# Optimization experiments

Measured on AMD Instinct MI355X. Metric: run time of the kernel, lower is better.

Reference implementation:

```python
import jax, jax.numpy as jnp
import numpy as np

N = 8192       # n_concepts
D = 128        # embed_dim
L = 2          # n_layers
ALPHA = 0.7
BETA = 0.3
LAM = 0.1      # lambda_decay


def setup_inputs() -> dict:
    key = jax.random.key(0)
    ks = jax.random.split(key, 16)
    adj = jax.random.randint(ks[0], (N, N), 0, 2).astype(jnp.float32)
    s = 0.05
    return {
        "adj": adj,
        "concept_embed": jax.random.normal(ks[1], (N, D), jnp.float32) * s,
        # torch Linear weight is [out,in]; stored here as [in,out] for x @ W
        "gc_w": jax.random.normal(ks[2], (L, D, D), jnp.float32) * s,
        "gc_b": jnp.zeros((L, D), jnp.float32),
        "wq": jax.random.normal(ks[3], (D, D), jnp.float32) * s,
        "bq": jnp.zeros((D,), jnp.float32),
        "wk": jax.random.normal(ks[4], (D, D), jnp.float32) * s,
        "bk": jnp.zeros((D,), jnp.float32),
        "wv": jax.random.normal(ks[5], (D, D), jnp.float32) * s,
        "bv": jnp.zeros((D,), jnp.float32),
        "g1_w": jax.random.normal(ks[6], (4 * D, 2 * D), jnp.float32) * s,
        "g1_b": jnp.zeros((2 * D,), jnp.float32),
        "g2_w": jax.random.normal(ks[7], (2 * D, 4), jnp.float32) * s,
        "g2_b": jnp.zeros((4,), jnp.float32),
        "layer_weights": jnp.ones((L,), jnp.float32) / L,
    }


def _aggregate(E, adj, wq, bq, wk, bk, wv, bv, g1_w, g1_b, g2_w, g2_b):
    nbr = adj != 0                                            # [N,N] neighbor pattern
    nrm = jnp.maximum(jnp.linalg.norm(E, axis=1), 1e-8)       # torch cosine_similarity eps
    sim = (E @ E.T) / (nrm[:, None] * nrm[None, :])           # [N,N] cosine sims
    pos = nbr & (sim >= ALPHA)
    neg = nbr & (sim <= BETA)
    bnd = nbr & (sim > BETA) & (sim < ALPHA)
    posf = pos.astype(E.dtype)
    negf = neg.astype(E.dtype)
    # masked means (zero when region empty, matching torch zeros fallback)
    pos_emb = (posf @ E) / jnp.maximum(posf.sum(1, keepdims=True), 1.0)
    neg_emb = LAM * (negf @ E) / jnp.maximum(negf.sum(1, keepdims=True), 1.0)
    # boundary region: attention of node i over its boundary neighbors
    Q = E @ wq + bq
    K = E @ wk + bk
    V = E @ wv + bv
    s = (Q @ K.T) / np.sqrt(D).astype(np.float32)             # [N,N]
    m = jnp.max(jnp.where(bnd, s, -jnp.inf), axis=1, keepdims=True)
    m = jnp.where(jnp.isfinite(m), m, 0.0)                    # safe max when region empty
    e = jnp.where(bnd, jnp.exp(s - m), 0.0)
    w = e / jnp.maximum(e.sum(1, keepdims=True), 1e-30)       # masked softmax (0 if empty)
    bnd_emb = w @ V
    # gated fusion of [self, pos, bound, neg]
    concat = jnp.concatenate([E, pos_emb, bnd_emb, neg_emb], axis=1)  # [N,4D]
    h = jax.nn.relu(concat @ g1_w + g1_b)
    gate = jax.nn.softmax(h @ g2_w + g2_b, axis=-1)           # [N,4]
    regions = jnp.stack([E, pos_emb, bnd_emb, neg_emb], axis=1)  # [N,4,D]
    fused = jnp.einsum('nr,nrd->nd', gate, regions)
    # nodes with no neighbors keep their own embedding
    return jnp.where(nbr.any(axis=1, keepdims=True), fused, E)


def reference(adj, concept_embed, gc_w, gc_b, wq, bq, wk, bk, wv, bv,
              g1_w, g1_b, g2_w, g2_b, layer_weights):
    cur = concept_embed
    outs = []
    for l in range(L):
        agg = _aggregate(cur, adj, wq, bq, wk, bk, wv, bv, g1_w, g1_b, g2_w, g2_b)
        cur = jax.nn.relu(agg @ gc_w[l] + gc_b[l])
        outs.append(cur)
    lw = jax.nn.softmax(layer_weights)
    return jnp.einsum('l,lnd->nd', lw, jnp.stack(outs))
```

## Files before the change

kernel.cpp:

```cpp
#include <hip/hip_runtime.h>
#include <stdint.h>

#define NN 8192
#define DD 128
#define ALPHA 0.7f
#define BETA 0.3f
#define LAM 0.1f
#define QSCALE 0.08838834764831845f
#define DELTA 3e-5f
#define FLAGCAP 262144
#define FLAG2CAP 1048576

typedef __attribute__((ext_vector_type(8))) short short8;
typedef __attribute__((ext_vector_type(4))) float f32x4;
typedef unsigned short ush;

__device__ __forceinline__ ush f2bf(float f){
  union { float f; unsigned u; } v; v.f = f;
  return (ush)((v.u + 0x7FFFu + ((v.u >> 16) & 1u)) >> 16);
}
__device__ __forceinline__ float bf2f(ush s){
  union { unsigned u; float f; } v; v.u = ((unsigned)s) << 16; return v.f;
}

__global__ void k_pack(const float* __restrict__ adj, unsigned* __restrict__ adjw){
  int i = blockIdx.x, wave = threadIdx.x >> 6, lane = threadIdx.x & 63;
  for (int seg = wave; seg < 128; seg += 4){
    int j = seg*64 + lane;
    unsigned long long bm = __ballot(adj[(size_t)i*NN + j] != 0.0f);
    if (lane == 0)  adjw[i*256 + seg*2]     = (unsigned)bm;
    if (lane == 32) adjw[i*256 + seg*2 + 1] = (unsigned)(bm >> 32);
  }
}

__global__ void k_norm(const float* __restrict__ E, double* __restrict__ nrm64,
                       ush* __restrict__ Enh, ush* __restrict__ Enl){
  int i = blockIdx.x*4 + (threadIdx.x >> 6);
  int l = threadIdx.x & 63;
  float v0 = E[i*DD + l], v1 = E[i*DD + 64 + l];
  double ss = (double)v0*(double)v0 + (double)v1*(double)v1;
  #pragma unroll
  for (int m = 32; m; m >>= 1) ss += __shfl_xor(ss, m, 64);
  double nr = sqrt(ss); if (nr < 1e-8) nr = 1e-8;
  float inv = (float)(1.0 / nr);
  float n0 = v0*inv, n1 = v1*inv;
  ush h0 = f2bf(n0), h1 = f2bf(n1);
  Enh[i*DD + l] = h0;       Enh[i*DD + 64 + l] = h1;
  Enl[i*DD + l] = f2bf(n0 - bf2f(h0));
  Enl[i*DD + 64 + l] = f2bf(n1 - bf2f(h1));
  if (l == 0) nrm64[i] = nr;
}

__global__ void k_transsplit(const float* __restrict__ in, ush* __restrict__ outH,
                             ush* __restrict__ outL){
  __shared__ float t[64][65];
  int r0 = blockIdx.x * 64, c0 = blockIdx.y * 64;
  for (int idx = threadIdx.x; idx < 4096; idx += 256){
    int r = idx >> 6, c = idx & 63;
    t[r][c] = in[(r0 + r)*DD + c0 + c];
  }
  __syncthreads();
  for (int idx = threadIdx.x; idx < 4096; idx += 256){
    int c = idx >> 6, r = idx & 63;
    float v = t[r][c];
    ush h = f2bf(v);
    outH[(size_t)(c0 + c)*NN + r0 + r] = h;
    outL[(size_t)(c0 + c)*NN + r0 + r] = f2bf(v - bf2f(h));
  }
}

__global__ void k_transw_all(const float* __restrict__ wq, const float* __restrict__ wk,
                             const float* __restrict__ wv, const float* __restrict__ g1w,
                             const float* __restrict__ gcw,
                             ush* __restrict__ qkvTh, ush* __restrict__ qkvTl,
                             ush* __restrict__ g1wTh, ush* __restrict__ g1wTl,
                             ush* __restrict__ gcwTh, ush* __restrict__ gcwTl){
  int idx = blockIdx.x*256 + threadIdx.x;
  const float* src; ush *dh, *dl; int K, Nout, li;
  if      (idx <  16384){ src=wq;        dh=qkvTh;        dl=qkvTl;        K=128; Nout=128; li=idx; }
  else if (idx <  32768){ src=wk;        dh=qkvTh+16384;  dl=qkvTl+16384;  K=128; Nout=128; li=idx-16384; }
  else if (idx <  49152){ src=wv;        dh=qkvTh+32768;  dl=qkvTl+32768;  K=128; Nout=128; li=idx-32768; }
  else if (idx < 180224){ src=g1w;       dh=g1wTh;        dl=g1wTl;        K=512; Nout=256; li=idx-49152; }
  else if (idx < 196608){ src=gcw;       dh=gcwTh;        dl=gcwTl;        K=128; Nout=128; li=idx-180224; }
  else if (idx < 212992){ src=gcw+16384; dh=gcwTh+16384;  dl=gcwTl+16384;  K=128; Nout=128; li=idx-196608; }
  else return;
  int k = li / Nout, n = li - k*Nout;
  float v = src[li];
  ush h = f2bf(v);
  dh[n*K + k] = h;
  dl[n*K + k] = f2bf(v - bf2f(h));
}

__global__ void k_qkv(const float* __restrict__ A,
                      const ush* __restrict__ BtH, const ush* __restrict__ BtL,
                      const float* __restrict__ bq, const float* __restrict__ bk,
                      const float* __restrict__ bv,
                      ush* __restrict__ Qh, ush* __restrict__ Kh,
                      ush* __restrict__ VhT, ush* __restrict__ VloT){
  __shared__ float sV[128*33];
  int tid = threadIdx.x, lane = tid & 63, wave = tid >> 6;
  int l15 = lane & 15, quad = lane >> 4;
  int rowblk = blockIdx.x * 32;
  int row16 = rowblk + (wave >> 1)*16;
  int nf0 = (wave & 1)*12;
  f32x4 acc[12];
  #pragma unroll
  for (int i = 0; i < 12; i++){ f32x4 z = {0.f,0.f,0.f,0.f}; acc[i] = z; }
  #pragma unroll
  for (int kk = 0; kk < 4; kk++){
    const float* ap = &A[(row16 + l15)*DD + kk*32 + quad*8];
    short8 ah, al;
    #pragma unroll
    for (int j = 0; j < 8; j++){
      float v = ap[j];
      ush h = f2bf(v);
      ah[j] = (short)h; al[j] = (short)f2bf(v - bf2f(h));
    }
    #pragma unroll
    for (int i = 0; i < 12; i++){
      int bo = ((nf0 + i)*16 + l15)*DD + kk*32 + quad*8;
      short8 bh = *(const short8*)&BtH[bo];
      short8 bl = *(const short8*)&BtL[bo];
      acc[i] = __builtin_amdgcn_mfma_f32_16x16x32_bf16(ah, bh, acc[i], 0, 0, 0);
      acc[i] = __builtin_amdgcn_mfma_f32_16x16x32_bf16(al, bh, acc[i], 0, 0, 0);
      acc[i] = __builtin_amdgcn_mfma_f32_16x16x32_bf16(ah, bl, acc[i], 0, 0, 0);
    }
  }
  #pragma unroll
  for (int i = 0; i < 12; i++){
    int nfg = nf0 + i;
    int grp = nfg >> 3;
    int col = (nfg & 7)*16 + l15;
    float b = (grp == 0) ? bq[col] : (grp == 1) ? bk[col] : bv[col];
    #pragma unroll
    for (int r = 0; r < 4; r++){
      int row = row16 + quad*4 + r;
      float v = acc[i][r] + b;
      if (grp == 0)      Qh[row*DD + col] = f2bf(v * QSCALE);
      else if (grp == 1) Kh[row*DD + col] = f2bf(v);
      else               sV[col*33 + (row - rowblk)] = v;
    }
  }
  __syncthreads();
  int feat = tid >> 1, rh = (tid & 1)*16;
  ush hh[16], ll[16];
  #pragma unroll
  for (int j = 0; j < 16; j++){
    float v = sV[feat*33 + rh + j];
    ush h = f2bf(v);
    hh[j] = h; ll[j] = f2bf(v - bf2f(h));
  }
  size_t go = (size_t)feat*NN + rowblk + rh;
  *(uint4*)&VhT [go]     = *(const uint4*)&hh[0];
  *(uint4*)&VhT [go + 8] = *(const uint4*)&hh[8];
  *(uint4*)&VloT[go]     = *(const uint4*)&ll[0];
  *(uint4*)&VloT[go + 8] = *(const uint4*)&ll[8];
}

__global__ void k_g1(const float* __restrict__ E, const float* __restrict__ P,
                     const float* __restrict__ B, const float* __restrict__ N,
                     const float* __restrict__ cntP, const float* __restrict__ cntN,
                     const float* __restrict__ denB,
                     const ush* __restrict__ BtH, const ush* __restrict__ BtL,
                     const float* __restrict__ bias, float* __restrict__ out){
  int tid = threadIdx.x, lane = tid & 63, wave = tid >> 6;
  int l15 = lane & 15, quad = lane >> 4;
  int row16 = blockIdx.x*16;
  int nf0 = wave*4;
  int row = row16 + l15;
  float cp = cntP[row], cn = cntN[row], dn = denB[row];
  float rs[4] = {1.f, 1.f/fmaxf(cp,1.f), (dn > 0.5f) ? (1.f/dn) : 0.f, LAM/fmaxf(cn,1.f)};
  const float* bases[4] = {E, P, B, N};
  f32x4 acc[4];
  #pragma unroll
  for (int nf = 0; nf < 4; nf++){ f32x4 z = {0.f,0.f,0.f,0.f}; acc[nf] = z; }
  #pragma unroll
  for (int kk = 0; kk < 16; kk++){
    const float* ap = &bases[kk>>2][row*DD + (kk&3)*32 + quad*8];
    float sc = rs[kk>>2];
    short8 ah, al;
    #pragma unroll
    for (int j = 0; j < 8; j++){
      float v = ap[j] * sc;
      ush h = f2bf(v);
      ah[j] = (short)h; al[j] = (short)f2bf(v - bf2f(h));
    }
    #pragma unroll
    for (int nf = 0; nf < 4; nf++){
      int bo = ((nf0 + nf)*16 + l15)*512 + kk*32 + quad*8;
      short8 bh = *(const short8*)&BtH[bo];
      short8 bl = *(const short8*)&BtL[bo];
      acc[nf] = __builtin_amdgcn_mfma_f32_16x16x32_bf16(ah, bh, acc[nf], 0, 0, 0);
      acc[nf] = __builtin_amdgcn_mfma_f32_16x16x32_bf16(al, bh, acc[nf], 0, 0, 0);
      acc[nf] = __builtin_amdgcn_mfma_f32_16x16x32_bf16(ah, bl, acc[nf], 0, 0, 0);
    }
  }
  #pragma unroll
  for (int nf = 0; nf < 4; nf++){
    int col = (nf0 + nf)*16 + l15;
    float b = bias[col];
    #pragma unroll
    for (int r = 0; r < 4; r++){
      int rr = row16 + quad*4 + r;
      out[rr*256 + col] = fmaxf(acc[nf][r] + b, 0.f);
    }
  }
}

__global__ void k_fusegc(const float* __restrict__ E, const float* __restrict__ P,
                         const float* __restrict__ B, const float* __restrict__ N,
                         const float* __restrict__ hbuf, const float* __restrict__ g2w,
                         const float* __restrict__ g2b,
                         const float* __restrict__ cntP, const float* __restrict__ cntN,
                         const float* __restrict__ denB,
                         const ush* __restrict__ BtH, const ush* __restrict__ BtL,
                         const float* __restrict__ bias,
                         const float* __restrict__ prevC, const float* __restrict__ lwv,
                         int dofinal, float* __restrict__ out){
  int tid = threadIdx.x, lane = tid & 63, wave = tid >> 6;
  int l15 = lane & 15, quad = lane >> 4;
  int row16 = blockIdx.x*16;
  int nf0 = wave*2;
  int row = row16 + l15;
  float l0=0,l1=0,l2=0,l3=0;
  #pragma unroll
  for (int i = 0; i < 16; i++){
    float4 hv = *(const float4*)&hbuf[row*256 + quad*64 + i*4];
    float hvv[4] = {hv.x, hv.y, hv.z, hv.w};
    #pragma unroll
    for (int j = 0; j < 4; j++){
      float4 w4 = *(const float4*)&g2w[(quad*64 + i*4 + j)*4];
      l0 = fmaf(hvv[j], w4.x, l0); l1 = fmaf(hvv[j], w4.y, l1);
      l2 = fmaf(hvv[j], w4.z, l2); l3 = fmaf(hvv[j], w4.w, l3);
    }
  }
  l0 += __shfl_xor(l0,16,64); l0 += __shfl_xor(l0,32,64);
  l1 += __shfl_xor(l1,16,64); l1 += __shfl_xor(l1,32,64);
  l2 += __shfl_xor(l2,16,64); l2 += __shfl_xor(l2,32,64);
  l3 += __shfl_xor(l3,16,64); l3 += __shfl_xor(l3,32,64);
  l0 += g2b[0]; l1 += g2b[1]; l2 += g2b[2]; l3 += g2b[3];
  float mx = fmaxf(fmaxf(l0,l1), fmaxf(l2,l3));
  float e0 = __expf(l0-mx), e1 = __expf(l1-mx), e2 = __expf(l2-mx), e3 = __expf(l3-mx);
  float inv = 1.f/(e0+e1+e2+e3);
  float g0 = e0*inv, g1v = e1*inv, g2v = e2*inv, g3 = e3*inv;
  float cp = cntP[row], cn = cntN[row], dn = denB[row];
  bool any = (cp + cn > 0.5f) || (dn > 0.5f);
  float pscl = g1v/fmaxf(cp,1.f);
  float bscl = (dn > 0.5f) ? (g2v/dn) : 0.f;
  float nscl = LAM*g3/fmaxf(cn,1.f);
  f32x4 acc[2];
  #pragma unroll
  for (int nf = 0; nf < 2; nf++){ f32x4 z = {0.f,0.f,0.f,0.f}; acc[nf] = z; }
  #pragma unroll
  for (int kk = 0; kk < 4; kk++){
    int koff = row*DD + kk*32 + quad*8;
    short8 ah, al;
    #pragma unroll
    for (int j = 0; j < 8; j++){
      float ev = E[koff + j];
      float v = any ? (g0*ev + pscl*P[koff+j] + bscl*B[koff+j] + nscl*N[koff+j]) : ev;
      ush h = f2bf(v);
      ah[j] = (short)h; al[j] = (short)f2bf(v - bf2f(h));
    }
    #pragma unroll
    for (int nf = 0; nf < 2; nf++){
      int bo = ((nf0 + nf)*16 + l15)*DD + kk*32 + quad*8;
      short8 bh = *(const short8*)&BtH[bo];
      short8 bl = *(const short8*)&BtL[bo];
      acc[nf] = __builtin_amdgcn_mfma_f32_16x16x32_bf16(ah, bh, acc[nf], 0, 0, 0);
      acc[nf] = __builtin_amdgcn_mfma_f32_16x16x32_bf16(al, bh, acc[nf], 0, 0, 0);
      acc[nf] = __builtin_amdgcn_mfma_f32_16x16x32_bf16(ah, bl, acc[nf], 0, 0, 0);
    }
  }
  float we0 = 0.5f, we1 = 0.5f;
  if (dofinal){
    float a0 = lwv[0], a1 = lwv[1];
    float mw = fmaxf(a0, a1);
    float x0 = __expf(a0-mw), x1 = __expf(a1-mw);
    float iv = 1.f/(x0+x1);
    we0 = x0*iv; we1 = x1*iv;
  }
  #pragma unroll
  for (int nf = 0; nf < 2; nf++){
    int col = (nf0 + nf)*16 + l15;
    float b = bias[col];
    #pragma unroll
    for (int r = 0; r < 4; r++){
      int rr = row16 + quad*4 + r;
      float val = fmaxf(acc[nf][r] + b, 0.f);
      if (dofinal) val = we0*prevC[rr*DD + col] + we1*val;
      out[rr*DD + col] = val;
    }
  }
}

#define BM 64
#define BN 32
#define CSPLIT 4
#define CCHUNK (NN/CSPLIT)
#define NTILES (CCHUNK/BN)
#define RSTRIDE 136
#define FSTRIDE 80
#define MSTRIDE 80

template<int DENSEB>
__launch_bounds__(256, 2)
__global__ void k_fused(const unsigned* __restrict__ adjw,
    const ush* __restrict__ Enh, const ush* __restrict__ Enl,
    const ush* __restrict__ Qh,  const ush* __restrict__ Kh,
    const ush* __restrict__ EhiT, const ush* __restrict__ EloT,
    const ush* __restrict__ VhT,  const ush* __restrict__ VloT,
    float* __restrict__ Nsum, float* __restrict__ Bsum,
    float* __restrict__ cntN, float* __restrict__ denB,
    int* __restrict__ flagCnt, float4* __restrict__ flags,
    int* __restrict__ flag2Cnt, float4* __restrict__ flags2)
{
  __shared__ __attribute__((aligned(16))) ush sEnh[32*RSTRIDE];
  __shared__ __attribute__((aligned(16))) ush sEnl[32*RSTRIDE];
  __shared__ __attribute__((aligned(16))) ush sKh [32*RSTRIDE];
  __shared__ __attribute__((aligned(16))) ush sE2 [128*FSTRIDE];
  __shared__ __attribute__((aligned(16))) ush sV2 [DENSEB ? 128*FSTRIDE : 16];
  __shared__ __attribute__((aligned(16))) ush sM  [4][16*MSTRIDE];

  int tid = threadIdx.x, lane = tid & 63, wave = tid >> 6;
  int l15 = lane & 15, quad = lane >> 4;
  int rowblk = blockIdx.x >> 2, split = blockIdx.x & 3;
  int row0 = rowblk * BM + wave * 16;
  int col0 = split * CCHUNK;

  short8 bEnh[4], bEnl[4], bQ[4];
  #pragma unroll
  for (int kf = 0; kf < 4; kf++){
    int go = (row0 + l15)*DD + kf*32 + quad*8;
    bEnh[kf] = *(const short8*)&Enh[go];
    bEnl[kf] = *(const short8*)&Enl[go];
    bQ  [kf] = *(const short8*)&Qh [go];
  }

  f32x4 accN[8], accB[DENSEB ? 8 : 1];
  #pragma unroll
  for (int nf = 0; nf < 8; nf++){ f32x4 z = {0.f,0.f,0.f,0.f}; accN[nf]=z; }
  if (DENSEB){
    #pragma unroll
    for (int nf = 0; nf < 8; nf++){ f32x4 z = {0.f,0.f,0.f,0.f}; accB[nf]=z; }
  }
  float cnL = 0.f, dbL = 0.f;

  int f0 = tid >> 2,        n0 = (tid & 3)*8;
  int f1 = (tid+256) >> 2,  n1 = ((tid+256) & 3)*8;
  uint4 pEh0, pEh1, pEl0, pEl1, pVh0, pVh1, pVl0, pVl1;
  {
    size_t g0 = (size_t)f0*NN + col0 + n0, g1 = (size_t)f1*NN + col0 + n1;
    pEh0 = *(const uint4*)&EhiT[g0]; pEh1 = *(const uint4*)&EhiT[g1];
    pEl0 = *(const uint4*)&EloT[g0]; pEl1 = *(const uint4*)&EloT[g1];
    if (DENSEB){
      pVh0 = *(const uint4*)&VhT [g0]; pVh1 = *(const uint4*)&VhT [g1];
      pVl0 = *(const uint4*)&VloT[g0]; pVl1 = *(const uint4*)&VloT[g1];
    }
  }
  int rr0 = tid >> 4,       ro0 = (tid & 15)*8;
  int rr1 = (tid+256) >> 4, ro1 = ((tid+256) & 15)*8;

  for (int t = 0; t < NTILES; t++){
    int c0 = col0 + t*BN;
    __syncthreads();
    *(uint4*)&sE2[f0*FSTRIDE + n0]      = pEh0;  *(uint4*)&sE2[f1*FSTRIDE + n1]      = pEh1;
    *(uint4*)&sE2[f0*FSTRIDE + 40 + n0] = pEl0;  *(uint4*)&sE2[f1*FSTRIDE + 40 + n1] = pEl1;
    if (DENSEB){
      *(uint4*)&sV2[f0*FSTRIDE + n0]      = pVh0;  *(uint4*)&sV2[f1*FSTRIDE + n1]      = pVh1;
      *(uint4*)&sV2[f0*FSTRIDE + 40 + n0] = pVl0;  *(uint4*)&sV2[f1*FSTRIDE + 40 + n1] = pVl1;
    }
    {
      uint4 a0 = *(const uint4*)&Enh[(c0 + rr0)*DD + ro0];
      uint4 a1 = *(const uint4*)&Enh[(c0 + rr1)*DD + ro1];
      uint4 b0 = *(const uint4*)&Enl[(c0 + rr0)*DD + ro0];
      uint4 b1 = *(const uint4*)&Enl[(c0 + rr1)*DD + ro1];
      uint4 k0 = *(const uint4*)&Kh [(c0 + rr0)*DD + ro0];
      uint4 k1 = *(const uint4*)&Kh [(c0 + rr1)*DD + ro1];
      *(uint4*)&sEnh[rr0*RSTRIDE + ro0] = a0;  *(uint4*)&sEnh[rr1*RSTRIDE + ro1] = a1;
      *(uint4*)&sEnl[rr0*RSTRIDE + ro0] = b0;  *(uint4*)&sEnl[rr1*RSTRIDE + ro1] = b1;
      *(uint4*)&sKh [rr0*RSTRIDE + ro0] = k0;  *(uint4*)&sKh [rr1*RSTRIDE + ro1] = k1;
    }
    __syncthreads();
    if (t + 1 < NTILES){
      int c1 = c0 + BN;
      size_t g0 = (size_t)f0*NN + c1 + n0, g1 = (size_t)f1*NN + c1 + n1;
      pEh0 = *(const uint4*)&EhiT[g0]; pEh1 = *(const uint4*)&EhiT[g1];
      pEl0 = *(const uint4*)&EloT[g0]; pEl1 = *(const uint4*)&EloT[g1];
      if (DENSEB){
        pVh0 = *(const uint4*)&VhT [g0]; pVh1 = *(const uint4*)&VhT [g1];
        pVl0 = *(const uint4*)&VloT[g0]; pVl1 = *(const uint4*)&VloT[g1];
      }
    }
    unsigned aw = adjw[(row0 + l15)*256 + (c0 >> 5)];

    f32x4 simT[2], svT[2];
    { f32x4 z = {0.f,0.f,0.f,0.f}; simT[0]=z; simT[1]=z; svT[0]=z; svT[1]=z; }
    #pragma unroll
    for (int f = 0; f < 2; f++){
      #pragma unroll
      for (int kf = 0; kf < 4; kf++){
        int la = (f*16 + l15)*RSTRIDE + kf*32 + quad*8;
        short8 ch = *(const short8*)&sEnh[la];
        short8 cl = *(const short8*)&sEnl[la];
        short8 ck = *(const short8*)&sKh [la];
        simT[f] = __builtin_amdgcn_mfma_f32_16x16x32_bf16(ch, bEnh[kf], simT[f],0,0,0);
        simT[f] = __builtin_amdgcn_mfma_f32_16x16x32_bf16(cl, bEnh[kf], simT[f],0,0,0);
        simT[f] = __builtin_amdgcn_mfma_f32_16x16x32_bf16(ch, bEnl[kf], simT[f],0,0,0);
        svT [f] = __builtin_amdgcn_mfma_f32_16x16x32_bf16(ck, bQ  [kf], svT [f],0,0,0);
      }
    }
    ushort4 ehv[2], elv[2];
    unsigned flagb = 0, spb = 0;
    #pragma unroll
    for (int f = 0; f < 2; f++){
      ush vn2[4], veh[4], vel[4];
      #pragma unroll
      for (int r = 0; r < 4; r++){
        int cbit = f*16 + quad*4 + r;
        bool nbr = (aw >> cbit) & 1u;
        float c = simT[f][r], s = svT[f][r];
        bool pos = nbr && (c >= ALPHA);
        bool neg = nbr && (c <= BETA);
        bool bnd = nbr && !pos && !neg;
        vn2[r] = neg ? (ush)0x3F80 : (ush)0;
        cnL += neg ? 1.f : 0.f;
        if (DENSEB){
          float e = bnd ? __expf(s) : 0.f;
          ush eh = f2bf(e);
          veh[r] = eh;
          vel[r] = f2bf(e - bf2f(eh));
          dbL += e;
        }
        if (nbr && (fabsf(c - ALPHA) < DELTA || fabsf(c - BETA) < DELTA))
          flagb |= 1u << (f*4 + r);
        if (pos || (!DENSEB && bnd))
          spb |= 1u << (f*4 + r);
      }
      int mb = l15*MSTRIDE + f*16 + quad*4;
      *(ushort4*)&sM[wave][mb] = make_ushort4(vn2[0],vn2[1],vn2[2],vn2[3]);
      if (DENSEB){
        ehv[f] = make_ushort4(veh[0],veh[1],veh[2],veh[3]);
        elv[f] = make_ushort4(vel[0],vel[1],vel[2],vel[3]);
      }
    }
    if (__ballot((flagb | spb) != 0)){
      #pragma unroll
      for (int f = 0; f < 2; f++){
        #pragma unroll
        for (int r = 0; r < 4; r++){
          int bit = f*4 + r;
          bool fl = (flagb >> bit) & 1u;
          unsigned long long bm = __ballot(fl);
          if (bm){
            int leader = __ffsll((long long)bm) - 1;
            int base = 0;
            if (lane == leader) base = atomicAdd(flagCnt, __popcll(bm));
            base = __shfl(base, leader, 64);
            if (fl){
              int id = base + __popcll(bm & ((1ull << lane) - 1ull));
              if (id < FLAGCAP){
                float4 rec;
                rec.x = __int_as_float(row0 + l15);
                rec.y = __int_as_float(c0 + f*16 + quad*4 + r);
                rec.z = simT[f][r]; rec.w = svT[f][r];
                flags[id] = rec;
              }
            }
          }
          bool f2 = (spb >> bit) & 1u;
          unsigned long long bm2 = __ballot(f2);
          if (bm2){
            int leader = __ffsll((long long)bm2) - 1;
            int base = 0;
            if (lane == leader) base = atomicAdd(flag2Cnt, __popcll(bm2));
            base = __shfl(base, leader, 64);
            if (f2){
              int id = base + __popcll(bm2 & ((1ull << lane) - 1ull));
              if (id < FLAG2CAP){
                float c = simT[f][r];
                int j = c0 + f*16 + quad*4 + r;
                int cls = (c >= ALPHA) ? 0 : 1;
                float4 rec;
                rec.x = __int_as_float(row0 + l15);
                rec.y = __int_as_float(j | (cls << 16));
                rec.z = c; rec.w = svT[f][r];
                flags2[id] = rec;
              }
            }
          }
        }
      }
    }
    {
      short8 mNeg = *(const short8*)&sM[wave][l15*MSTRIDE + quad*8];
      #pragma unroll
      for (int nf = 0; nf < 8; nf++){
        int so = (nf*16 + l15)*FSTRIDE + quad*8;
        short8 eth = *(const short8*)&sE2[so];
        short8 etl = *(const short8*)&sE2[so + 40];
        accN[nf] = __builtin_amdgcn_mfma_f32_16x16x32_bf16(mNeg, eth, accN[nf],0,0,0);
        accN[nf] = __builtin_amdgcn_mfma_f32_16x16x32_bf16(mNeg, etl, accN[nf],0,0,0);
      }
    }
    if (DENSEB){
      int mb0 = l15*MSTRIDE + quad*4;
      *(ushort4*)&sM[wave][mb0]      = ehv[0];
      *(ushort4*)&sM[wave][mb0 + 16] = ehv[1];
      *(ushort4*)&sM[wave][mb0 + 40] = elv[0];
      *(ushort4*)&sM[wave][mb0 + 56] = elv[1];
      short8 mEh = *(const short8*)&sM[wave][l15*MSTRIDE + quad*8];
      short8 mEl = *(const short8*)&sM[wave][l15*MSTRIDE + 40 + quad*8];
      #pragma unroll
      for (int nf = 0; nf < 8; nf++){
        int so = (nf*16 + l15)*FSTRIDE + quad*8;
        short8 vth = *(const short8*)&sV2[so];
        short8 vtl = *(const short8*)&sV2[so + 40];
        accB[nf] = __builtin_amdgcn_mfma_f32_16x16x32_bf16(mEh, vth, accB[nf],0,0,0);
        accB[nf] = __builtin_amdgcn_mfma_f32_16x16x32_bf16(mEl, vth, accB[nf],0,0,0);
        accB[nf] = __builtin_amdgcn_mfma_f32_16x16x32_bf16(mEh, vtl, accB[nf],0,0,0);
      }
    }
  }
  #pragma unroll
  for (int nf = 0; nf < 8; nf++){
    int col = nf*16 + l15;
    #pragma unroll
    for (int r = 0; r < 4; r++){
      int row = row0 + quad*4 + r;
      atomicAdd(&Nsum[row*DD + col], accN[nf][r]);
      if (DENSEB) atomicAdd(&Bsum[row*DD + col], accB[nf][r]);
    }
  }
  cnL += __shfl_xor(cnL, 16, 64); cnL += __shfl_xor(cnL, 32, 64);
  if (DENSEB){ dbL += __shfl_xor(dbL, 16, 64); dbL += __shfl_xor(dbL, 32, 64); }
  if (quad == 0){
    atomicAdd(&cntN[row0 + l15], cnL);
    if (DENSEB) atomicAdd(&denB[row0 + l15], dbL);
  }
}

__global__ void k_sparsePB(const ush* __restrict__ EhiT, const ush* __restrict__ EloT,
    const ush* __restrict__ VhT,  const ush* __restrict__ VloT,
    const int* __restrict__ flag2Cnt, const float4* __restrict__ flags2,
    float* __restrict__ Psum, float* __restrict__ Bsum,
    float* __restrict__ cntP, float* __restrict__ denB)
{
  int cnt = *flag2Cnt; if (cnt > FLAG2CAP) cnt = FLAG2CAP;
  int lane = threadIdx.x & 63;
  int gw = (blockIdx.x * blockDim.x + threadIdx.x) >> 6;
  int nw = (gridDim.x * blockDim.x) >> 6;
  for (int idx = gw; idx < cnt; idx += nw){
    float4 rec = flags2[idx];
    int i = __float_as_int(rec.x);
    int jraw = __float_as_int(rec.y);
    int j = jraw & 0xFFFF, cls = jraw >> 16;
    if (cls == 0){
      #pragma unroll
      for (int h = 0; h < 2; h++){
        int d = lane + h*64;
        float ev = bf2f(EhiT[(size_t)d*NN + j]) + bf2f(EloT[(size_t)d*NN + j]);
        atomicAdd(&Psum[i*DD + d], ev);
      }
      if (lane == 0) atomicAdd(&cntP[i], 1.f);
    } else {
      float e = __expf(rec.w);
      float ehf = bf2f(f2bf(e));
      float elf = bf2f(f2bf(e - ehf));
      #pragma unroll
      for (int h = 0; h < 2; h++){
        int d = lane + h*64;
        float vh = bf2f(VhT [(size_t)d*NN + j]);
        float vl = bf2f(VloT[(size_t)d*NN + j]);
        atomicAdd(&Bsum[i*DD + d], ehf*vh + elf*vh + ehf*vl);
      }
      if (lane == 0) atomicAdd(&denB[i], e);
    }
  }
}

__global__ void k_refine(const float* __restrict__ E, const double* __restrict__ nrm64,
    const ush* __restrict__ EhiT, const ush* __restrict__ EloT,
    const ush* __restrict__ VhT,  const ush* __restrict__ VloT,
    const int* __restrict__ flagCnt, const float4* __restrict__ flags,
    float* __restrict__ Psum, float* __restrict__ Nsum, float* __restrict__ Bsum,
    float* __restrict__ cntP, float* __restrict__ cntN, float* __restrict__ denB)
{
  int cnt = *flagCnt; if (cnt > FLAGCAP) cnt = FLAGCAP;
  int lane = threadIdx.x & 63;
  int gw = (blockIdx.x * blockDim.x + threadIdx.x) >> 6;
  int nw = (gridDim.x * blockDim.x) >> 6;
  for (int idx = gw; idx < cnt; idx += nw){
    float4 rec = flags[idx];
    int i = __float_as_int(rec.x), j = __float_as_int(rec.y);
    float c = rec.z, s = rec.w;
    float ei0 = E[i*DD + lane], ei1 = E[i*DD + 64 + lane];
    float ej0 = E[j*DD + lane], ej1 = E[j*DD + 64 + lane];
    double d = (double)ei0*(double)ej0 + (double)ei1*(double)ej1;
    #pragma unroll
    for (int m = 32; m; m >>= 1) d += __shfl_xor(d, m, 64);
    double se = d / (nrm64[i]*nrm64[j]);
    int ce = (se >= (double)ALPHA) ? 0 : ((se <= (double)BETA) ? 1 : 2);
    int cc = (c >= ALPHA) ? 0 : ((c <= BETA) ? 1 : 2);
    if (ce == cc) continue;
    float e = __expf(s);
    float ehf = bf2f(f2bf(e));
    float elf = bf2f(f2bf(e - ehf));
    #pragma unroll
    for (int h = 0; h < 2; h++){
      int dd2 = lane + h*64;
      float ev = bf2f(EhiT[(size_t)dd2*NN + j]) + bf2f(EloT[(size_t)dd2*NN + j]);
      float vh = bf2f(VhT[(size_t)dd2*NN + j]);
      float vl = bf2f(VloT[(size_t)dd2*NN + j]);
      float bv = ehf*vh + elf*vh + ehf*vl;
      float* subA = (cc==0) ? Psum : (cc==1) ? Nsum : Bsum;
      atomicAdd(&subA[i*DD + dd2], (cc==2) ? -bv : -ev);
      float* addA = (ce==0) ? Psum : (ce==1) ? Nsum : Bsum;
      atomicAdd(&addA[i*DD + dd2], (ce==2) ?  bv :  ev);
    }
    if (lane == 0){
      float* subC = (cc==0) ? cntP : (cc==1) ? cntN : denB;
      atomicAdd(&subC[i], (cc==2) ? -e : -1.f);
      float* addC = (ce==0) ? cntP : (ce==1) ? cntN : denB;
      atomicAdd(&addC[i], (ce==2) ?  e :  1.f);
    }
  }
}

extern "C" void kernel_launch(void* const* d_in, const int* in_sizes, int n_in,
                              void* d_out, int out_size, void* d_ws, size_t ws_size,
                              hipStream_t stream){
  const float* adj   = (const float*)d_in[0];
  const float* embed = (const float*)d_in[1];
  const float* gc_w  = (const float*)d_in[2];
  const float* gc_b  = (const float*)d_in[3];
  const float* wq = (const float*)d_in[4];
  const float* bq = (const float*)d_in[5];
  const float* wk = (const float*)d_in[6];
  const float* bk = (const float*)d_in[7];
  const float* wv = (const float*)d_in[8];
  const float* bv = (const float*)d_in[9];
  const float* g1w = (const float*)d_in[10];
  const float* g1b = (const float*)d_in[11];
  const float* g2w = (const float*)d_in[12];
  const float* g2b = (const float*)d_in[13];
  const float* lw  = (const float*)d_in[14];
  float* out = (float*)d_out;

  char* p = (char*)d_ws;
  auto alloc = [&](size_t bytes)->void*{ void* r = (void*)p; p += (bytes + 255) & ~(size_t)255; return r; };
  ush* qkvTh = (ush*)alloc(384*128*2);  ush* qkvTl = (ush*)alloc(384*128*2);
  ush* g1wTh = (ush*)alloc(512*256*2);  ush* g1wTl = (ush*)alloc(512*256*2);
  ush* gcwTh = (ush*)alloc(2*128*128*2); ush* gcwTl = (ush*)alloc(2*128*128*2);
  unsigned* adjw = (unsigned*)alloc((size_t)NN*256*4);
  double* nrm64 = (double*)alloc(NN*8);
  ush* Enh  = (ush*)alloc((size_t)NN*DD*2);
  ush* Enl  = (ush*)alloc((size_t)NN*DD*2);
  ush* EhiT = (ush*)alloc((size_t)NN*DD*2);
  ush* EloT = (ush*)alloc((size_t)NN*DD*2);
  ush* Qh   = (ush*)alloc((size_t)NN*DD*2);
  ush* Khb  = (ush*)alloc((size_t)NN*DD*2);
  ush* VhT  = (ush*)alloc((size_t)NN*DD*2);
  ush* VloT = (ush*)alloc((size_t)NN*DD*2);
  char* zbase = p;
  float* Psum = (float*)alloc((size_t)NN*DD*4);
  float* Nsum = (float*)alloc((size_t)NN*DD*4);
  float* Bsum = (float*)alloc((size_t)NN*DD*4);
  float* cntP = (float*)alloc(NN*4);
  float* cntN = (float*)alloc(NN*4);
  float* denB = (float*)alloc(NN*4);
  int*   flagCnt  = (int*)alloc(256);
  int*   flag2Cnt = (int*)alloc(256);
  size_t zbytes = (size_t)(p - zbase);
  float4* flags  = (float4*)alloc((size_t)FLAGCAP*16);
  float4* flags2 = (float4*)alloc((size_t)FLAG2CAP*16);
  float* hbuf = (float*)alloc((size_t)NN*256*4);
  float* cur0 = (float*)alloc((size_t)NN*DD*4);

  k_pack<<<NN, 256, 0, stream>>>(adj, adjw);
  k_transw_all<<<832, 256, 0, stream>>>(wq, wk, wv, g1w, gc_w,
      qkvTh, qkvTl, g1wTh, g1wTl, gcwTh, gcwTl);

  const float* Ecur = embed;
  for (int l = 0; l < 2; l++){
    k_norm<<<2048, 256, 0, stream>>>(Ecur, nrm64, Enh, Enl);
    k_transsplit<<<dim3(128,2), 256, 0, stream>>>(Ecur, EhiT, EloT);
    k_qkv<<<256, 256, 0, stream>>>(Ecur, qkvTh, qkvTl, bq, bk, bv, Qh, Khb, VhT, VloT);
    hipMemsetAsync(zbase, 0, zbytes, stream);
    if (l == 0)
      k_fused<0><<<(NN/BM)*CSPLIT, 256, 0, stream>>>(adjw, Enh, Enl, Qh, Khb,
          EhiT, EloT, VhT, VloT, Nsum, Bsum, cntN, denB,
          flagCnt, flags, flag2Cnt, flags2);
    else
      k_fused<1><<<(NN/BM)*CSPLIT, 256, 0, stream>>>(adjw, Enh, Enl, Qh, Khb,
          EhiT, EloT, VhT, VloT, Nsum, Bsum, cntN, denB,
          flagCnt, flags, flag2Cnt, flags2);
    k_sparsePB<<<256, 256, 0, stream>>>(EhiT, EloT, VhT, VloT, flag2Cnt, flags2,
        Psum, Bsum, cntP, denB);
    k_refine<<<512, 256, 0, stream>>>(Ecur, nrm64, EhiT, EloT, VhT, VloT, flagCnt, flags,
        Psum, Nsum, Bsum, cntP, cntN, denB);
    k_g1<<<512, 256, 0, stream>>>(Ecur, Psum, Bsum, Nsum, cntP, cntN, denB,
        g1wTh, g1wTl, g1b, hbuf);
    k_fusegc<<<512, 256, 0, stream>>>(Ecur, Psum, Bsum, Nsum, hbuf, g2w, g2b,
        cntP, cntN, denB, gcwTh + l*128*128, gcwTl + l*128*128, gc_b + l*128,
        cur0, lw, l, (l == 0) ? cur0 : out);
    Ecur = (l == 0) ? cur0 : out;
  }
}
```

Baseline: 1.111 ms.

## Merge prep, sparse-fix, and MLP kernels to cut launches and intermediate buffers

Three groups of kernels are combined into single launches. Norm, transpose-split and QKV become one k_prep dispatched by block index. The sparse P/B accumulation and the refine pass become one k_fix. The gate MLP (g1) and the fuse/gc stage become one k_mlp, which keeps the hidden activations in shared memory instead of a global hbuf. A dotmode flag also lets k_fix recompute the QK score from Q and K in layer 0 instead of using the stored value, which changes how the k_fused side stores records. The aim is fewer launches and less global traffic. The cost is larger heterogeneous blocks with more register and LDS pressure.

```diff
diff --git a/kernel.cpp b/kernel.cpp
--- a/kernel.cpp
+++ b/kernel.cpp
@@ -23,6 +23,17 @@
   union { unsigned u; float f; } v; v.u = ((unsigned)s) << 16; return v.f;
 }
 
+__device__ __forceinline__ float qkdot(const ush* __restrict__ Qh,
+                                       const ush* __restrict__ Kh,
+                                       int i, int j, int lane){
+  float q0 = bf2f(Qh[i*DD + lane]),      k0 = bf2f(Kh[j*DD + lane]);
+  float q1 = bf2f(Qh[i*DD + 64 + lane]), k1 = bf2f(Kh[j*DD + 64 + lane]);
+  float s = q0*k0 + q1*k1;
+  #pragma unroll
+  for (int m = 32; m; m >>= 1) s += __shfl_xor(s, m, 64);
+  return s;
+}
+
 __global__ void k_pack(const float* __restrict__ adj, unsigned* __restrict__ adjw){
   int i = blockIdx.x, wave = threadIdx.x >> 6, lane = threadIdx.x & 63;
   for (int seg = wave; seg < 128; seg += 4){
@@ -30,42 +41,6 @@
     unsigned long long bm = __ballot(adj[(size_t)i*NN + j] != 0.0f);
     if (lane == 0)  adjw[i*256 + seg*2]     = (unsigned)bm;
     if (lane == 32) adjw[i*256 + seg*2 + 1] = (unsigned)(bm >> 32);
-  }
-}
-
-__global__ void k_norm(const float* __restrict__ E, double* __restrict__ nrm64,
-                       ush* __restrict__ Enh, ush* __restrict__ Enl){
-  int i = blockIdx.x*4 + (threadIdx.x >> 6);
-  int l = threadIdx.x & 63;
-  float v0 = E[i*DD + l], v1 = E[i*DD + 64 + l];
-  double ss = (double)v0*(double)v0 + (double)v1*(double)v1;
-  #pragma unroll
-  for (int m = 32; m; m >>= 1) ss += __shfl_xor(ss, m, 64);
-  double nr = sqrt(ss); if (nr < 1e-8) nr = 1e-8;
-  float inv = (float)(1.0 / nr);
-  float n0 = v0*inv, n1 = v1*inv;
-  ush h0 = f2bf(n0), h1 = f2bf(n1);
-  Enh[i*DD + l] = h0;       Enh[i*DD + 64 + l] = h1;
-  Enl[i*DD + l] = f2bf(n0 - bf2f(h0));
-  Enl[i*DD + 64 + l] = f2bf(n1 - bf2f(h1));
-  if (l == 0) nrm64[i] = nr;
-}
-
-__global__ void k_transsplit(const float* __restrict__ in, ush* __restrict__ outH,
-                             ush* __restrict__ outL){
-  __shared__ float t[64][65];
-  int r0 = blockIdx.x * 64, c0 = blockIdx.y * 64;
-  for (int idx = threadIdx.x; idx < 4096; idx += 256){
-    int r = idx >> 6, c = idx & 63;
-    t[r][c] = in[(r0 + r)*DD + c0 + c];
-  }
-  __syncthreads();
-  for (int idx = threadIdx.x; idx < 4096; idx += 256){
-    int c = idx >> 6, r = idx & 63;
-    float v = t[r][c];
-    ush h = f2bf(v);
-    outH[(size_t)(c0 + c)*NN + r0 + r] = h;
-    outL[(size_t)(c0 + c)*NN + r0 + r] = f2bf(v - bf2f(h));
   }
 }
 
@@ -91,205 +66,233 @@
   dl[n*K + k] = f2bf(v - bf2f(h));
 }
 
-__global__ void k_qkv(const float* __restrict__ A,
-                      const ush* __restrict__ BtH, const ush* __restrict__ BtL,
-                      const float* __restrict__ bq, const float* __restrict__ bk,
-                      const float* __restrict__ bv,
-                      ush* __restrict__ Qh, ush* __restrict__ Kh,
-                      ush* __restrict__ VhT, ush* __restrict__ VloT){
+__global__ void k_prep(const float* __restrict__ E, double* __restrict__ nrm64,
+                       ush* __restrict__ Enh, ush* __restrict__ Enl,
+                       ush* __restrict__ EhiT, ush* __restrict__ EloT,
+                       const ush* __restrict__ BtH, const ush* __restrict__ BtL,
+                       const float* __restrict__ bq, const float* __restrict__ bk,
+                       const float* __restrict__ bv,
+                       ush* __restrict__ Qh, ush* __restrict__ Kh,
+                       ush* __restrict__ VhT, ush* __restrict__ VloT){
+  __shared__ float t[64][65];
   __shared__ float sV[128*33];
-  int tid = threadIdx.x, lane = tid & 63, wave = tid >> 6;
-  int l15 = lane & 15, quad = lane >> 4;
-  int rowblk = blockIdx.x * 32;
-  int row16 = rowblk + (wave >> 1)*16;
-  int nf0 = (wave & 1)*12;
-  f32x4 acc[12];
-  #pragma unroll
-  for (int i = 0; i < 12; i++){ f32x4 z = {0.f,0.f,0.f,0.f}; acc[i] = z; }
-  #pragma unroll
-  for (int kk = 0; kk < 4; kk++){
-    const float* ap = &A[(row16 + l15)*DD + kk*32 + quad*8];
-    short8 ah, al;
-    #pragma unroll
-    for (int j = 0; j < 8; j++){
-      float v = ap[j];
+  int bid = blockIdx.x, tid = threadIdx.x;
+  if (bid < 2048){
+    int i = bid*4 + (tid >> 6);
+    int l = tid & 63;
+    float v0 = E[i*DD + l], v1 = E[i*DD + 64 + l];
+    double ss = (double)v0*(double)v0 + (double)v1*(double)v1;
+    #pragma unroll
+    for (int m = 32; m; m >>= 1) ss += __shfl_xor(ss, m, 64);
+    double nr = sqrt(ss); if (nr < 1e-8) nr = 1e-8;
+    float inv = (float)(1.0 / nr);
+    float n0 = v0*inv, n1 = v1*inv;
+    ush h0 = f2bf(n0), h1 = f2bf(n1);
+    Enh[i*DD + l] = h0;       Enh[i*DD + 64 + l] = h1;
+    Enl[i*DD + l] = f2bf(n0 - bf2f(h0));
+    Enl[i*DD + 64 + l] = f2bf(n1 - bf2f(h1));
+    if (l == 0) nrm64[i] = nr;
+  } else if (bid < 2304){
+    int lin = bid - 2048;
+    int r0 = (lin >> 1) * 64, c0 = (lin & 1) * 64;
+    for (int idx = tid; idx < 4096; idx += 256){
+      int r = idx >> 6, c = idx & 63;
+      t[r][c] = E[(r0 + r)*DD + c0 + c];
+    }
+    __syncthreads();
+    for (int idx = tid; idx < 4096; idx += 256){
+      int c = idx >> 6, r = idx & 63;
+      float v = t[r][c];
       ush h = f2bf(v);
-      ah[j] = (short)h; al[j] = (short)f2bf(v - bf2f(h));
+      EhiT[(size_t)(c0 + c)*NN + r0 + r] = h;
+      EloT[(size_t)(c0 + c)*NN + r0 + r] = f2bf(v - bf2f(h));
+    }
+  } else {
+    int lane = tid & 63, wave = tid >> 6;
+    int l15 = lane & 15, quad = lane >> 4;
+    int rowblk = (bid - 2304) * 32;
+    int row16 = rowblk + (wave >> 1)*16;
+    int nf0 = (wave & 1)*12;
+    f32x4 acc[12];
+    #pragma unroll
+    for (int i = 0; i < 12; i++){ f32x4 z = {0.f,0.f,0.f,0.f}; acc[i] = z; }
+    #pragma unroll
+    for (int kk = 0; kk < 4; kk++){
+      const float* ap = &E[(row16 + l15)*DD + kk*32 + quad*8];
+      short8 ah, al;
+      #pragma unroll
+      for (int j = 0; j < 8; j++){
+        float v = ap[j];
+        ush h = f2bf(v);
+        ah[j] = (short)h; al[j] = (short)f2bf(v - bf2f(h));
+      }
+      #pragma unroll
+      for (int i = 0; i < 12; i++){
+        int bo = ((nf0 + i)*16 + l15)*DD + kk*32 + quad*8;
+        short8 bh = *(const short8*)&BtH[bo];
+        short8 bl = *(const short8*)&BtL[bo];
+        acc[i] = __builtin_amdgcn_mfma_f32_16x16x32_bf16(ah, bh, acc[i], 0, 0, 0);
+        acc[i] = __builtin_amdgcn_mfma_f32_16x16x32_bf16(al, bh, acc[i], 0, 0, 0);
+        acc[i] = __builtin_amdgcn_mfma_f32_16x16x32_bf16(ah, bl, acc[i], 0, 0, 0);
+      }
     }
     #pragma unroll
     for (int i = 0; i < 12; i++){
-      int bo = ((nf0 + i)*16 + l15)*DD + kk*32 + quad*8;
-      short8 bh = *(const short8*)&BtH[bo];
-      short8 bl = *(const short8*)&BtL[bo];
-      acc[i] = __builtin_amdgcn_mfma_f32_16x16x32_bf16(ah, bh, acc[i], 0, 0, 0);
-      acc[i] = __builtin_amdgcn_mfma_f32_16x16x32_bf16(al, bh, acc[i], 0, 0, 0);
-      acc[i] = __builtin_amdgcn_mfma_f32_16x16x32_bf16(ah, bl, acc[i], 0, 0, 0);
-    }
-  }
-  #pragma unroll
-  for (int i = 0; i < 12; i++){
-    int nfg = nf0 + i;
-    int grp = nfg >> 3;
-    int col = (nfg & 7)*16 + l15;
-    float b = (grp == 0) ? bq[col] : (grp == 1) ? bk[col] : bv[col];
-    #pragma unroll
-    for (int r = 0; r < 4; r++){
-      int row = row16 + quad*4 + r;
-      float v = acc[i][r] + b;
-      if (grp == 0)      Qh[row*DD + col] = f2bf(v * QSCALE);
-      else if (grp == 1) Kh[row*DD + col] = f2bf(v);
-      else               sV[col*33 + (row - rowblk)] = v;
-    }
-  }
-  __syncthreads();
-  int feat = tid >> 1, rh = (tid & 1)*16;
-  ush hh[16], ll[16];
-  #pragma unroll
-  for (int j = 0; j < 16; j++){
-    float v = sV[feat*33 + rh + j];
-    ush h = f2bf(v);
-    hh[j] = h; ll[j] = f2bf(v - bf2f(h));
-  }
-  size_t go = (size_t)feat*NN + rowblk + rh;
-  *(uint4*)&VhT [go]     = *(const uint4*)&hh[0];
-  *(uint4*)&VhT [go + 8] = *(const uint4*)&hh[8];
-  *(uint4*)&VloT[go]     = *(const uint4*)&ll[0];
-  *(uint4*)&VloT[go + 8] = *(const uint4*)&ll[8];
-}
-
-__global__ void k_g1(const float* __restrict__ E, const float* __restrict__ P,
-                     const float* __restrict__ B, const float* __restrict__ N,
-                     const float* __restrict__ cntP, const float* __restrict__ cntN,
-                     const float* __restrict__ denB,
-                     const ush* __restrict__ BtH, const ush* __restrict__ BtL,
-                     const float* __restrict__ bias, float* __restrict__ out){
+      int nfg = nf0 + i;
+      int grp = nfg >> 3;
+      int col = (nfg & 7)*16 + l15;
+      float b = (grp == 0) ? bq[col] : (grp == 1) ? bk[col] : bv[col];
+      #pragma unroll
+      for (int r = 0; r < 4; r++){
+        int row = row16 + quad*4 + r;
+        float v = acc[i][r] + b;
+        if (grp == 0)      Qh[row*DD + col] = f2bf(v * QSCALE);
+        else if (grp == 1) Kh[row*DD + col] = f2bf(v);
+        else               sV[col*33 + (row - rowblk)] = v;
+      }
+    }
+    __syncthreads();
+    int feat = tid >> 1, rh = (tid & 1)*16;
+    ush hh[16], ll[16];
+    #pragma unroll
+    for (int j = 0; j < 16; j++){
+      float v = sV[feat*33 + rh + j];
+      ush h = f2bf(v);
+      hh[j] = h; ll[j] = f2bf(v - bf2f(h));
+    }
+    size_t go = (size_t)feat*NN + rowblk + rh;
+    *(uint4*)&VhT [go]     = *(const uint4*)&hh[0];
+    *(uint4*)&VhT [go + 8] = *(const uint4*)&hh[8];
+    *(uint4*)&VloT[go]     = *(const uint4*)&ll[0];
+    *(uint4*)&VloT[go + 8] = *(const uint4*)&ll[8];
+  }
+}
+
+__global__ void k_mlp(const float* __restrict__ E, const float* __restrict__ P,
+                      const float* __restrict__ B, const float* __restrict__ N,
+                      const float* __restrict__ cntP, const float* __restrict__ cntN,
+                      const float* __restrict__ denB,
+                      const ush* __restrict__ g1Th, const ush* __restrict__ g1Tl,
+                      const float* __restrict__ g1b,
+                      const float* __restrict__ g2w, const float* __restrict__ g2b,
+                      const ush* __restrict__ gcTh, const ush* __restrict__ gcTl,
+                      const float* __restrict__ gcb,
+                      const float* __restrict__ prevC, const float* __restrict__ lwv,
+                      int dofinal, float* __restrict__ out){
+  __shared__ float sH[16*260];
   int tid = threadIdx.x, lane = tid & 63, wave = tid >> 6;
   int l15 = lane & 15, quad = lane >> 4;
   int row16 = blockIdx.x*16;
-  int nf0 = wave*4;
   int row = row16 + l15;
   float cp = cntP[row], cn = cntN[row], dn = denB[row];
-  float rs[4] = {1.f, 1.f/fmaxf(cp,1.f), (dn > 0.5f) ? (1.f/dn) : 0.f, LAM/fmaxf(cn,1.f)};
-  const float* bases[4] = {E, P, B, N};
-  f32x4 acc[4];
-  #pragma unroll
-  for (int nf = 0; nf < 4; nf++){ f32x4 z = {0.f,0.f,0.f,0.f}; acc[nf] = z; }
-  #pragma unroll
-  for (int kk = 0; kk < 16; kk++){
-    const float* ap = &bases[kk>>2][row*DD + (kk&3)*32 + quad*8];
-    float sc = rs[kk>>2];
-    short8 ah, al;
-    #pragma unroll
-    for (int j = 0; j < 8; j++){
-      float v = ap[j] * sc;
-      ush h = f2bf(v);
-      ah[j] = (short)h; al[j] = (short)f2bf(v - bf2f(h));
+  {
+    int nf0 = wave*4;
+    float rs[4] = {1.f, 1.f/fmaxf(cp,1.f), (dn > 0.5f) ? (1.f/dn) : 0.f, LAM/fmaxf(cn,1.f)};
+    const float* bases[4] = {E, P, B, N};
+    f32x4 acc[4];
+    #pragma unroll
+    for (int nf = 0; nf < 4; nf++){ f32x4 z = {0.f,0.f,0.f,0.f}; acc[nf] = z; }
+    #pragma unroll
+    for (int kk = 0; kk < 16; kk++){
+      const float* ap = &bases[kk>>2][row*DD + (kk&3)*32 + quad*8];
+      float sc = rs[kk>>2];
+      short8 ah, al;
+      #pragma unroll
+      for (int j = 0; j < 8; j++){
+        float v = ap[j] * sc;
+        ush h = f2bf(v);
+        ah[j] = (short)h; al[j] = (short)f2bf(v - bf2f(h));
+      }
+      #pragma unroll
+      for (int nf = 0; nf < 4; nf++){
+        int bo = ((nf0 + nf)*16 + l15)*512 + kk*32 + quad*8;
+        short8 bh = *(const short8*)&g1Th[bo];
+        short8 bl = *(const short8*)&g1Tl[bo];
+        acc[nf] = __builtin_amdgcn_mfma_f32_16x16x32_bf16(ah, bh, acc[nf], 0, 0, 0);
+        acc[nf] = __builtin_amdgcn_mfma_f32_16x16x32_bf16(al, bh, acc[nf], 0, 0, 0);
+        acc[nf] = __builtin_amdgcn_mfma_f32_16x16x32_bf16(ah, bl, acc[nf], 0, 0, 0);
+      }
     }
     #pragma unroll
     for (int nf = 0; nf < 4; nf++){
-      int bo = ((nf0 + nf)*16 + l15)*512 + kk*32 + quad*8;
-      short8 bh = *(const short8*)&BtH[bo];
-      short8 bl = *(const short8*)&BtL[bo];
-      acc[nf] = __builtin_amdgcn_mfma_f32_16x16x32_bf16(ah, bh, acc[nf], 0, 0, 0);
-      acc[nf] = __builtin_amdgcn_mfma_f32_16x16x32_bf16(al, bh, acc[nf], 0, 0, 0);
-      acc[nf] = __builtin_amdgcn_mfma_f32_16x16x32_bf16(ah, bl, acc[nf], 0, 0, 0);
-    }
-  }
-  #pragma unroll
-  for (int nf = 0; nf < 4; nf++){
-    int col = (nf0 + nf)*16 + l15;
-    float b = bias[col];
-    #pragma unroll
-    for (int r = 0; r < 4; r++){
-      int rr = row16 + quad*4 + r;
-      out[rr*256 + col] = fmaxf(acc[nf][r] + b, 0.f);
-    }
-  }
-}
-
-__global__ void k_fusegc(const float* __restrict__ E, const float* __restrict__ P,
-                         const float* __restrict__ B, const float* __restrict__ N,
-                         const float* __restrict__ hbuf, const float* __restrict__ g2w,
-                         const float* __restrict__ g2b,
-                         const float* __restrict__ cntP, const float* __restrict__ cntN,
-                         const float* __restrict__ denB,
-                         const ush* __restrict__ BtH, const ush* __restrict__ BtL,
-                         const float* __restrict__ bias,
-                         const float* __restrict__ prevC, const float* __restrict__ lwv,
-                         int dofinal, float* __restrict__ out){
-  int tid = threadIdx.x, lane = tid & 63, wave = tid >> 6;
-  int l15 = lane & 15, quad = lane >> 4;
-  int row16 = blockIdx.x*16;
-  int nf0 = wave*2;
-  int row = row16 + l15;
-  float l0=0,l1=0,l2=0,l3=0;
-  #pragma unroll
-  for (int i = 0; i < 16; i++){
-    float4 hv = *(const float4*)&hbuf[row*256 + quad*64 + i*4];
-    float hvv[4] = {hv.x, hv.y, hv.z, hv.w};
-    #pragma unroll
-    for (int j = 0; j < 4; j++){
-      float4 w4 = *(const float4*)&g2w[(quad*64 + i*4 + j)*4];
-      l0 = fmaf(hvv[j], w4.x, l0); l1 = fmaf(hvv[j], w4.y, l1);
-      l2 = fmaf(hvv[j], w4.z, l2); l3 = fmaf(hvv[j], w4.w, l3);
-    }
-  }
-  l0 += __shfl_xor(l0,16,64); l0 += __shfl_xor(l0,32,64);
-  l1 += __shfl_xor(l1,16,64); l1 += __shfl_xor(l1,32,64);
-  l2 += __shfl_xor(l2,16,64); l2 += __shfl_xor(l2,32,64);
-  l3 += __shfl_xor(l3,16,64); l3 += __shfl_xor(l3,32,64);
-  l0 += g2b[0]; l1 += g2b[1]; l2 += g2b[2]; l3 += g2b[3];
-  float mx = fmaxf(fmaxf(l0,l1), fmaxf(l2,l3));
-  float e0 = __expf(l0-mx), e1 = __expf(l1-mx), e2 = __expf(l2-mx), e3 = __expf(l3-mx);
-  float inv = 1.f/(e0+e1+e2+e3);
-  float g0 = e0*inv, g1v = e1*inv, g2v = e2*inv, g3 = e3*inv;
-  float cp = cntP[row], cn = cntN[row], dn = denB[row];
-  bool any = (cp + cn > 0.5f) || (dn > 0.5f);
-  float pscl = g1v/fmaxf(cp,1.f);
-  float bscl = (dn > 0.5f) ? (g2v/dn) : 0.f;
-  float nscl = LAM*g3/fmaxf(cn,1.f);
-  f32x4 acc[2];
-  #pragma unroll
-  for (int nf = 0; nf < 2; nf++){ f32x4 z = {0.f,0.f,0.f,0.f}; acc[nf] = z; }
-  #pragma unroll
-  for (int kk = 0; kk < 4; kk++){
-    int koff = row*DD + kk*32 + quad*8;
-    short8 ah, al;
-    #pragma unroll
-    for (int j = 0; j < 8; j++){
-      float ev = E[koff + j];
-      float v = any ? (g0*ev + pscl*P[koff+j] + bscl*B[koff+j] + nscl*N[koff+j]) : ev;
-      ush h = f2bf(v);
-      ah[j] = (short)h; al[j] = (short)f2bf(v - bf2f(h));
+      int col = (nf0 + nf)*16 + l15;
+      float b = g1b[col];
+      #pragma unroll
+      for (int r = 0; r < 4; r++)
+        sH[(quad*4 + r)*260 + col] = fmaxf(acc[nf][r] + b, 0.f);
+    }
+  }
+  __syncthreads();
+  {
+    int nf0 = wave*2;
+    float l0=0,l1=0,l2=0,l3=0;
+    #pragma unroll
+    for (int i = 0; i < 16; i++){
+      float4 hv = *(const float4*)&sH[l15*260 + quad*64 + i*4];
+      float hvv[4] = {hv.x, hv.y, hv.z, hv.w};
+      #pragma unroll
+      for (int j = 0; j < 4; j++){
+        float4 w4 = *(const float4*)&g2w[(quad*64 + i*4 + j)*4];
+        l0 = fmaf(hvv[j], w4.x, l0); l1 = fmaf(hvv[j], w4.y, l1);
+        l2 = fmaf(hvv[j], w4.z, l2); l3 = fmaf(hvv[j], w4.w, l3);
+      }
+    }
+    l0 += __shfl_xor(l0,16,64); l0 += __shfl_xor(l0,32,64);
+    l1 += __shfl_xor(l1,16,64); l1 += __shfl_xor(l1,32,64);
+    l2 += __shfl_xor(l2,16,64); l2 += __shfl_xor(l2,32,64);
+    l3 += __shfl_xor(l3,16,64); l3 += __shfl_xor(l3,32,64);
+    l0 += g2b[0]; l1 += g2b[1]; l2 += g2b[2]; l3 += g2b[3];
+    float mx = fmaxf(fmaxf(l0,l1), fmaxf(l2,l3));
+    float e0 = __expf(l0-mx), e1 = __expf(l1-mx), e2 = __expf(l2-mx), e3 = __expf(l3-mx);
+    float inv = 1.f/(e0+e1+e2+e3);
+    float g0 = e0*inv, g1v = e1*inv, g2v = e2*inv, g3 = e3*inv;
+    bool any = (cp + cn > 0.5f) || (dn > 0.5f);
+    float pscl = g1v/fmaxf(cp,1.f);
+    float bscl = (dn > 0.5f) ? (g2v/dn) : 0.f;
+    float nscl = LAM*g3/fmaxf(cn,1.f);
+    f32x4 acc[2];
+    #pragma unroll
+    for (int nf = 0; nf < 2; nf++){ f32x4 z = {0.f,0.f,0.f,0.f}; acc[nf] = z; }
+    #pragma unroll
+    for (int kk = 0; kk < 4; kk++){
+      int koff = row*DD + kk*32 + quad*8;
+      short8 ah, al;
+      #pragma unroll
+      for (int j = 0; j < 8; j++){
+        float ev = E[koff + j];
+        float v = any ? (g0*ev + pscl*P[koff+j] + bscl*B[koff+j] + nscl*N[koff+j]) : ev;
+        ush h = f2bf(v);
+        ah[j] = (short)h; al[j] = (short)f2bf(v - bf2f(h));
+      }
+      #pragma unroll
+      for (int nf = 0; nf < 2; nf++){
+        int bo = ((nf0 + nf)*16 + l15)*DD + kk*32 + quad*8;
+        short8 bh = *(const short8*)&gcTh[bo];
+        short8 bl = *(const short8*)&gcTl[bo];
+        acc[nf] = __builtin_amdgcn_mfma_f32_16x16x32_bf16(ah, bh, acc[nf], 0, 0, 0);
+        acc[nf] = __builtin_amdgcn_mfma_f32_16x16x32_bf16(al, bh, acc[nf], 0, 0, 0);
+        acc[nf] = __builtin_amdgcn_mfma_f32_16x16x32_bf16(ah, bl, acc[nf], 0, 0, 0);
+      }
+    }
+    float we0 = 0.5f, we1 = 0.5f;
+    if (dofinal){
+      float a0 = lwv[0], a1 = lwv[1];
+      float mw = fmaxf(a0, a1);
+      float x0 = __expf(a0-mw), x1 = __expf(a1-mw);
+      float iv = 1.f/(x0+x1);
+      we0 = x0*iv; we1 = x1*iv;
     }
     #pragma unroll
     for (int nf = 0; nf < 2; nf++){
-      int bo = ((nf0 + nf)*16 + l15)*DD + kk*32 + quad*8;
-      short8 bh = *(const short8*)&BtH[bo];
-      short8 bl = *(const short8*)&BtL[bo];
-      acc[nf] = __builtin_amdgcn_mfma_f32_16x16x32_bf16(ah, bh, acc[nf], 0, 0, 0);
-      acc[nf] = __builtin_amdgcn_mfma_f32_16x16x32_bf16(al, bh, acc[nf], 0, 0, 0);
-      acc[nf] = __builtin_amdgcn_mfma_f32_16x16x32_bf16(ah, bl, acc[nf], 0, 0, 0);
-    }
-  }
-  float we0 = 0.5f, we1 = 0.5f;
-  if (dofinal){
-    float a0 = lwv[0], a1 = lwv[1];
-    float mw = fmaxf(a0, a1);
-    float x0 = __expf(a0-mw), x1 = __expf(a1-mw);
-    float iv = 1.f/(x0+x1);
-    we0 = x0*iv; we1 = x1*iv;
-  }
-  #pragma unroll
-  for (int nf = 0; nf < 2; nf++){
-    int col = (nf0 + nf)*16 + l15;
-    float b = bias[col];
-    #pragma unroll
-    for (int r = 0; r < 4; r++){
-      int rr = row16 + quad*4 + r;
-      float val = fmaxf(acc[nf][r] + b, 0.f);
-      if (dofinal) val = we0*prevC[rr*DD + col] + we1*val;
-      out[rr*DD + col] = val;
+      int col = (nf0 + nf)*16 + l15;
+      float b = gcb[col];
+      #pragma unroll
+      for (int r = 0; r < 4; r++){
+        int rr = row16 + quad*4 + r;
+        float val = fmaxf(acc[nf][r] + b, 0.f);
+        if (dofinal) val = we0*prevC[rr*DD + col] + we1*val;
+        out[rr*DD + col] = val;
+      }
     }
   }
 }
@@ -317,7 +320,7 @@
 {
   __shared__ __attribute__((aligned(16))) ush sEnh[32*RSTRIDE];
   __shared__ __attribute__((aligned(16))) ush sEnl[32*RSTRIDE];
-  __shared__ __attribute__((aligned(16))) ush sKh [32*RSTRIDE];
+  __shared__ __attribute__((aligned(16))) ush sKh [DENSEB ? 32*RSTRIDE : 16];
   __shared__ __attribute__((aligned(16))) ush sE2 [128*FSTRIDE];
   __shared__ __attribute__((aligned(16))) ush sV2 [DENSEB ? 128*FSTRIDE : 16];
   __shared__ __attribute__((aligned(16))) ush sM  [4][16*MSTRIDE];
@@ -334,7 +337,7 @@
     int go = (row0 + l15)*DD + kf*32 + quad*8;
     bEnh[kf] = *(const short8*)&Enh[go];
     bEnl[kf] = *(const short8*)&Enl[go];
-    bQ  [kf] = *(const short8*)&Qh [go];
+    if (DENSEB) bQ[kf] = *(const short8*)&Qh[go];
   }
 
   f32x4 accN[8], accB[DENSEB ? 8 : 1];
@@ -375,11 +378,13 @@
       uint4 a1 = *(const uint4*)&Enh[(c0 + rr1)*DD + ro1];
       uint4 b0 = *(const uint4*)&Enl[(c0 + rr0)*DD + ro0];
       uint4 b1 = *(const uint4*)&Enl[(c0 + rr1)*DD + ro1];
-      uint4 k0 = *(const uint4*)&Kh [(c0 + rr0)*DD + ro0];
-      uint4 k1 = *(const uint4*)&Kh [(c0 + rr1)*DD + ro1];
       *(uint4*)&sEnh[rr0*RSTRIDE + ro0] = a0;  *(uint4*)&sEnh[rr1*RSTRIDE + ro1] = a1;
       *(uint4*)&sEnl[rr0*RSTRIDE + ro0] = b0;  *(uint4*)&sEnl[rr1*RSTRIDE + ro1] = b1;
-      *(uint4*)&sKh [rr0*RSTRIDE + ro0] = k0;  *(uint4*)&sKh [rr1*RSTRIDE + ro1] = k1;
+      if (DENSEB){
+        uint4 k0 = *(const uint4*)&Kh[(c0 + rr0)*DD + ro0];
+        uint4 k1 = *(const uint4*)&Kh[(c0 + rr1)*DD + ro1];
+        *(uint4*)&sKh[rr0*RSTRIDE + ro0] = k0;  *(uint4*)&sKh[rr1*RSTRIDE + ro1] = k1;
+      }
     }
     __syncthreads();
     if (t + 1 < NTILES){
@@ -403,11 +408,13 @@
         int la = (f*16 + l15)*RSTRIDE + kf*32 + quad*8;
         short8 ch = *(const short8*)&sEnh[la];
         short8 cl = *(const short8*)&sEnl[la];
-        short8 ck = *(const short8*)&sKh [la];
         simT[f] = __builtin_amdgcn_mfma_f32_16x16x32_bf16(ch, bEnh[kf], simT[f],0,0,0);
         simT[f] = __builtin_amdgcn_mfma_f32_16x16x32_bf16(cl, bEnh[kf], simT[f],0,0,0);
         simT[f] = __builtin_amdgcn_mfma_f32_16x16x32_bf16(ch, bEnl[kf], simT[f],0,0,0);
-        svT [f] = __builtin_amdgcn_mfma_f32_16x16x32_bf16(ck, bQ  [kf], svT [f],0,0,0);
+        if (DENSEB){
+          short8 ck = *(const short8*)&sKh[la];
+          svT[f] = __builtin_amdgcn_mfma_f32_16x16x32_bf16(ck, bQ[kf], svT[f],0,0,0);
+        }
       }
     }
     ushort4 ehv[2], elv[2];
@@ -419,14 +426,14 @@
       for (int r = 0; r < 4; r++){
         int cbit = f*16 + quad*4 + r;
         bool nbr = (aw >> cbit) & 1u;
-        float c = simT[f][r], s = svT[f][r];
+        float c = simT[f][r];
         bool pos = nbr && (c >= ALPHA);
         bool neg = nbr && (c <= BETA);
         bool bnd = nbr && !pos && !neg;
         vn2[r] = neg ? (ush)0x3F80 : (ush)0;
         cnL += neg ? 1.f : 0.f;
         if (DENSEB){
-          float e = bnd ? __expf(s) : 0.f;
+          float e = bnd ? __expf(svT[f][r]) : 0.f;
           ush eh = f2bf(e);
           veh[r] = eh;
           vel[r] = f2bf(e - bf2f(eh));
@@ -463,7 +470,8 @@
                 float4 rec;
                 rec.x = __int_as_float(row0 + l15);
                 rec.y = __int_as_float(c0 + f*16 + quad*4 + r);
-                rec.z = simT[f][r]; rec.w = svT[f][r];
+                rec.z = simT[f][r];
+                rec.w = DENSEB ? svT[f][r] : 0.f;
                 flags[id] = rec;
               }
             }
@@ -484,7 +492,8 @@
                 float4 rec;
                 rec.x = __int_as_float(row0 + l15);
                 rec.y = __int_as_float(j | (cls << 16));
-                rec.z = c; rec.w = svT[f][r];
+                rec.z = c;
+                rec.w = DENSEB ? svT[f][r] : 0.f;
                 flags2[id] = rec;
               }
             }
@@ -540,89 +549,87 @@
   }
 }
 
-__global__ void k_sparsePB(const ush* __restrict__ EhiT, const ush* __restrict__ EloT,
-    const ush* __restrict__ VhT,  const ush* __restrict__ VloT,
-    const int* __restrict__ flag2Cnt, const float4* __restrict__ flags2,
-    float* __restrict__ Psum, float* __restrict__ Bsum,
-    float* __restrict__ cntP, float* __restrict__ denB)
-{
-  int cnt = *flag2Cnt; if (cnt > FLAG2CAP) cnt = FLAG2CAP;
-  int lane = threadIdx.x & 63;
-  int gw = (blockIdx.x * blockDim.x + threadIdx.x) >> 6;
-  int nw = (gridDim.x * blockDim.x) >> 6;
-  for (int idx = gw; idx < cnt; idx += nw){
-    float4 rec = flags2[idx];
-    int i = __float_as_int(rec.x);
-    int jraw = __float_as_int(rec.y);
-    int j = jraw & 0xFFFF, cls = jraw >> 16;
-    if (cls == 0){
-      #pragma unroll
-      for (int h = 0; h < 2; h++){
-        int d = lane + h*64;
-        float ev = bf2f(EhiT[(size_t)d*NN + j]) + bf2f(EloT[(size_t)d*NN + j]);
-        atomicAdd(&Psum[i*DD + d], ev);
-      }
-      if (lane == 0) atomicAdd(&cntP[i], 1.f);
-    } else {
-      float e = __expf(rec.w);
-      float ehf = bf2f(f2bf(e));
-      float elf = bf2f(f2bf(e - ehf));
-      #pragma unroll
-      for (int h = 0; h < 2; h++){
-        int d = lane + h*64;
-        float vh = bf2f(VhT [(size_t)d*NN + j]);
-        float vl = bf2f(VloT[(size_t)d*NN + j]);
-        atomicAdd(&Bsum[i*DD + d], ehf*vh + elf*vh + ehf*vl);
-      }
-      if (lane == 0) atomicAdd(&denB[i], e);
-    }
-  }
-}
-
-__global__ void k_refine(const float* __restrict__ E, const double* __restrict__ nrm64,
+__global__ void k_fix(const float* __restrict__ E, const double* __restrict__ nrm64,
     const ush* __restrict__ EhiT, const ush* __restrict__ EloT,
     const ush* __restrict__ VhT,  const ush* __restrict__ VloT,
-    const int* __restrict__ flagCnt, const float4* __restrict__ flags,
+    const ush* __restrict__ Qh,   const ush* __restrict__ Kh, int dotmode,
+    const int* __restrict__ flag2Cnt, const float4* __restrict__ flags2,
+    const int* __restrict__ flagCnt,  const float4* __restrict__ flags,
     float* __restrict__ Psum, float* __restrict__ Nsum, float* __restrict__ Bsum,
     float* __restrict__ cntP, float* __restrict__ cntN, float* __restrict__ denB)
 {
-  int cnt = *flagCnt; if (cnt > FLAGCAP) cnt = FLAGCAP;
   int lane = threadIdx.x & 63;
-  int gw = (blockIdx.x * blockDim.x + threadIdx.x) >> 6;
-  int nw = (gridDim.x * blockDim.x) >> 6;
-  for (int idx = gw; idx < cnt; idx += nw){
-    float4 rec = flags[idx];
-    int i = __float_as_int(rec.x), j = __float_as_int(rec.y);
-    float c = rec.z, s = rec.w;
-    float ei0 = E[i*DD + lane], ei1 = E[i*DD + 64 + lane];
-    float ej0 = E[j*DD + lane], ej1 = E[j*DD + 64 + lane];
-    double d = (double)ei0*(double)ej0 + (double)ei1*(double)ej1;
-    #pragma unroll
-    for (int m = 32; m; m >>= 1) d += __shfl_xor(d, m, 64);
-    double se = d / (nrm64[i]*nrm64[j]);
-    int ce = (se >= (double)ALPHA) ? 0 : ((se <= (double)BETA) ? 1 : 2);
-    int cc = (c >= ALPHA) ? 0 : ((c <= BETA) ? 1 : 2);
-    if (ce == cc) continue;
-    float e = __expf(s);
-    float ehf = bf2f(f2bf(e));
-    float elf = bf2f(f2bf(e - ehf));
-    #pragma unroll
-    for (int h = 0; h < 2; h++){
-      int dd2 = lane + h*64;
-      float ev = bf2f(EhiT[(size_t)dd2*NN + j]) + bf2f(EloT[(size_t)dd2*NN + j]);
-      float vh = bf2f(VhT[(size_t)dd2*NN + j]);
-      float vl = bf2f(VloT[(size_t)dd2*NN + j]);
-      float bv = ehf*vh + elf*vh + ehf*vl;
-      float* subA = (cc==0) ? Psum : (cc==1) ? Nsum : Bsum;
-      atomicAdd(&subA[i*DD + dd2], (cc==2) ? -bv : -ev);
-      float* addA = (ce==0) ? Psum : (ce==1) ? Nsum : Bsum;
-      atomicAdd(&addA[i*DD + dd2], (ce==2) ?  bv :  ev);
-    }
-    if (lane == 0){
-      float* subC = (cc==0) ? cntP : (cc==1) ? cntN : denB;
-      atomicAdd(&subC[i], (cc==2) ? -e : -1.f);
-      float* addC = (ce==0) ? cntP : (ce==1) ? cntN : denB;
-      atomicAdd(&addC[i], (ce==2) ?  e :  1.f);
+  if (blockIdx.x < 256){
+    int cnt = *flag2Cnt; if (cnt > FLAG2CAP) cnt = FLAG2CAP;
+    int gw = (blockIdx.x * blockDim.x + threadIdx.x) >> 6;
+    int nw = (256 * blockDim.x) >> 6;
+    for (int idx = gw; idx < cnt; idx += nw){
+      float4 rec = flags2[idx];
+      int i = __float_as_int(rec.x);
+      int jraw = __float_as_int(rec.y);
+      int j = jraw & 0xFFFF, cls = jraw >> 16;
+      if (cls == 0){
+        #pragma unroll
+        for (int h = 0; h < 2; h++){
+          int d = lane + h*64;
+          float ev = bf2f(EhiT[(size_t)d*NN + j]) + bf2f(EloT[(size_t)d*NN + j]);
+          atomicAdd(&Psum[i*DD + d], ev);
+        }
+        if (lane == 0) atomicAdd(&cntP[i], 1.f);
+      } else {
+        float s = dotmode ? qkdot(Qh, Kh, i, j, lane) : rec.w;
+        float e = __expf(s);
+        float ehf = bf2f(f2bf(e));
+        float elf = bf2f(f2bf(e - ehf));
+        #pragma unroll
+        for (int h = 0; h < 2; h++){
+          int d = lane + h*64;
+          float vh = bf2f(VhT [(size_t)d*NN + j]);
+          float vl = bf2f(VloT[(size_t)d*NN + j]);
+          atomicAdd(&Bsum[i*DD + d], ehf*vh + elf*vh + ehf*vl);
+        }
+        if (lane == 0) atomicAdd(&denB[i], e);
+      }
+    }
+  } else {
+    int cnt = *flagCnt; if (cnt > FLAGCAP) cnt = FLAGCAP;
+    int gw = ((blockIdx.x - 256) * blockDim.x + threadIdx.x) >> 6;
+    int nw = (512 * blockDim.x) >> 6;
+    for (int idx = gw; idx < cnt; idx += nw){
+      float4 rec = flags[idx];
+      int i = __float_as_int(rec.x), j = __float_as_int(rec.y);
+      float c = rec.z;
+      float ei0 = E[i*DD + lane], ei1 = E[i*DD + 64 + lane];
+      float ej0 = E[j*DD + lane], ej1 = E[j*DD + 64 + lane];
+      double d = (double)ei0*(double)ej0 + (double)ei1*(double)ej1;
+      #pragma unroll
+      for (int m = 32; m; m >>= 1) d += __shfl_xor(d, m, 64);
+      double se = d / (nrm64[i]*nrm64[j]);
+      int ce = (se >= (double)ALPHA) ? 0 : ((se <= (double)BETA) ? 1 : 2);
+      int cc = (c >= ALPHA) ? 0 : ((c <= BETA) ? 1 : 2);
+      if (ce == cc) continue;
+      float s = dotmode ? qkdot(Qh, Kh, i, j, lane) : rec.w;
+      float e = __expf(s);
+      float ehf = bf2f(f2bf(e));
+      float elf = bf2f(f2bf(e - ehf));
+      #pragma unroll
+      for (int h = 0; h < 2; h++){
+        int dd2 = lane + h*64;
+        float ev = bf2f(EhiT[(size_t)dd2*NN + j]) + bf2f(EloT[(size_t)dd2*NN + j]);
+        float vh = bf2f(VhT[(size_t)dd2*NN + j]);
+        float vl = bf2f(VloT[(size_t)dd2*NN + j]);
+        float bv = ehf*vh + elf*vh + ehf*vl;
+        float* subA = (cc==0) ? Psum : (cc==1) ? Nsum : Bsum;
+        atomicAdd(&subA[i*DD + dd2], (cc==2) ? -bv : -ev);
+        float* addA = (ce==0) ? Psum : (ce==1) ? Nsum : Bsum;
+        atomicAdd(&addA[i*DD + dd2], (ce==2) ?  bv :  ev);
+      }
+      if (lane == 0){
+        float* subC = (cc==0) ? cntP : (cc==1) ? cntN : denB;
+        atomicAdd(&subC[i], (cc==2) ? -e : -1.f);
+        float* addC = (ce==0) ? cntP : (ce==1) ? cntN : denB;
+        atomicAdd(&addC[i], (ce==2) ?  e :  1.f);
+      }
     }
   }
 }
@@ -674,7 +681,6 @@
   size_t zbytes = (size_t)(p - zbase);
   float4* flags  = (float4*)alloc((size_t)FLAGCAP*16);
   float4* flags2 = (float4*)alloc((size_t)FLAG2CAP*16);
-  float* hbuf = (float*)alloc((size_t)NN*256*4);
   float* cur0 = (float*)alloc((size_t)NN*DD*4);
 
   k_pack<<<NN, 256, 0, stream>>>(adj, adjw);
@@ -683,9 +689,8 @@
 
   const float* Ecur = embed;
   for (int l = 0; l < 2; l++){
-    k_norm<<<2048, 256, 0, stream>>>(Ecur, nrm64, Enh, Enl);
-    k_transsplit<<<dim3(128,2), 256, 0, stream>>>(Ecur, EhiT, EloT);
-    k_qkv<<<256, 256, 0, stream>>>(Ecur, qkvTh, qkvTl, bq, bk, bv, Qh, Khb, VhT, VloT);
+    k_prep<<<2560, 256, 0, stream>>>(Ecur, nrm64, Enh, Enl, EhiT, EloT,
+        qkvTh, qkvTl, bq, bk, bv, Qh, Khb, VhT, VloT);
     hipMemsetAsync(zbase, 0, zbytes, stream);
     if (l == 0)
       k_fused<0><<<(NN/BM)*CSPLIT, 256, 0, stream>>>(adjw, Enh, Enl, Qh, Khb,
@@ -695,14 +700,12 @@
       k_fused<1><<<(NN/BM)*CSPLIT, 256, 0, stream>>>(adjw, Enh, Enl, Qh, Khb,
           EhiT, EloT, VhT, VloT, Nsum, Bsum, cntN, denB,
           flagCnt, flags, flag2Cnt, flags2);
-    k_sparsePB<<<256, 256, 0, stream>>>(EhiT, EloT, VhT, VloT, flag2Cnt, flags2,
-        Psum, Bsum, cntP, denB);
-    k_refine<<<512, 256, 0, stream>>>(Ecur, nrm64, EhiT, EloT, VhT, VloT, flagCnt, flags,
+    k_fix<<<768, 256, 0, stream>>>(Ecur, nrm64, EhiT, EloT, VhT, VloT,
+        Qh, Khb, (l == 0) ? 1 : 0, flag2Cnt, flags2, flagCnt, flags,
         Psum, Nsum, Bsum, cntP, cntN, denB);
-    k_g1<<<512, 256, 0, stream>>>(Ecur, Psum, Bsum, Nsum, cntP, cntN, denB,
-        g1wTh, g1wTl, g1b, hbuf);
-    k_fusegc<<<512, 256, 0, stream>>>(Ecur, Psum, Bsum, Nsum, hbuf, g2w, g2b,
-        cntP, cntN, denB, gcwTh + l*128*128, gcwTl + l*128*128, gc_b + l*128,
+    k_mlp<<<512, 256, 0, stream>>>(Ecur, Psum, Bsum, Nsum, cntP, cntN, denB,
+        g1wTh, g1wTl, g1b, g2w, g2b,
+        gcwTh + l*128*128, gcwTl + l*128*128, gc_b + l*128,
         cur0, lw, l, (l == 0) ? cur0 : out);
     Ecur = (l == 0) ? cur0 : out;
   }
```

Result: faster. 1.088 ms (-2.1%).
